# Performance work log

Measured on AMD Instinct MI355X. Metric: run time of the kernel, lower is better.

The kernel has to match this reference:

```python
import jax, jax.numpy as jnp
import numpy as np

ALPHA = 0.2  # LeakyReLU negative slope
NEG_INF = -9e15  # matches torch -9000000000000000.0


def setup_inputs() -> dict:
    key = jax.random.key(0)
    k1, k2, k3, k4, k5, k6 = jax.random.split(key, 6)
    N, F_in, F_out = 4096, 512, 256
    adj = jax.random.randint(k1, (N, N), 0, 2, dtype=jnp.int32)
    h = jax.random.normal(k2, (N, F_in), dtype=jnp.float32)
    # proj: Linear(F_in, F_out)
    W = jax.random.normal(k3, (F_in, F_out), dtype=jnp.float32) * (1.0 / np.sqrt(F_in))
    b = jax.random.normal(k4, (F_out,), dtype=jnp.float32) * 0.01
    # proj_a: Linear(2*F_out, 1) split into the two halves acting on src/dst features
    a1 = jax.random.normal(k5, (F_out,), dtype=jnp.float32) * (1.0 / np.sqrt(2 * F_out))
    a2 = jax.random.normal(k6, (F_out,), dtype=jnp.float32) * (1.0 / np.sqrt(2 * F_out))
    a_b = jnp.zeros((), dtype=jnp.float32)
    return {"adj": adj, "h": h, "W": W, "b": b, "a1": a1, "a2": a2, "a_b": a_b}


def reference(adj, h, W, b, a1, a2, a_b):
    # wh = proj(h): [N, F_out]
    wh = h @ W + b
    # Fused form of the N x N x 2F concat + Linear(2F,1):
    # logits[i, j] = wh[i] . a1 + wh[j] . a2 + a_b
    f_src = wh @ a1  # [N]
    f_dst = wh @ a2  # [N]
    e = jax.nn.leaky_relu(f_src[:, None] + f_dst[None, :] + a_b, negative_slope=ALPHA)
    e = jnp.where(adj > 0, e, NEG_INF)
    att = jax.nn.softmax(e, axis=-1)  # F.softmax legacy dim=1 for 2D
    # dropout: inference mode (no-op) for deterministic reference
    out = att @ wh  # [N, F_out]
    return jax.nn.elu(out)  # concat=True
```

## Files before the change

### kernel.cpp

```cpp
#include <hip/hip_runtime.h>

#define NN   4096
#define FIN  512
#define FOUT 256
#define ALPHA 0.2f

typedef __attribute__((ext_vector_type(8))) short short8;
typedef __attribute__((ext_vector_type(4))) float f32x4;
typedef unsigned short u16;

__device__ __forceinline__ u16 f2bf(float x) {
    union { float f; unsigned u; } v; v.f = x;
    unsigned r = v.u + 0x7FFF + ((v.u >> 16) & 1);
    return (u16)(r >> 16);
}

__global__ __launch_bounds__(256) void k_wt(const float* __restrict__ W,
                                            u16* __restrict__ Wt) {
    __shared__ float s[64 * 65];
    const int t  = threadIdx.x;
    const int f0 = blockIdx.x * 64;
    const int k0 = blockIdx.y * 64;
    #pragma unroll
    for (int p = 0; p < 4; ++p) {
        int q = t + 256 * p, rr = q >> 4, cc = q & 15;
        float4 w4 = *(const float4*)&W[(size_t)(k0 + rr) * FOUT + f0 + cc * 4];
        s[(cc * 4 + 0) * 65 + rr] = w4.x;
        s[(cc * 4 + 1) * 65 + rr] = w4.y;
        s[(cc * 4 + 2) * 65 + rr] = w4.z;
        s[(cc * 4 + 3) * 65 + rr] = w4.w;
    }
    __syncthreads();
    #pragma unroll
    for (int p = 0; p < 4; ++p) {
        int q = t + 256 * p, f = q >> 4, kg = q & 15;
        ushort4 o;
        o.x = f2bf(s[f * 65 + kg * 4 + 0]);
        o.y = f2bf(s[f * 65 + kg * 4 + 1]);
        o.z = f2bf(s[f * 65 + kg * 4 + 2]);
        o.w = f2bf(s[f * 65 + kg * 4 + 3]);
        *(ushort4*)&Wt[(size_t)(f0 + f) * FIN + k0 + kg * 4] = o;
    }
}

__global__ __launch_bounds__(256) void k_proj(const float* __restrict__ h,
                                              const u16* __restrict__ Wt,
                                              const float* __restrict__ bias,
                                              float* __restrict__ wh) {
    __shared__ u16 s_h[32 * 40];
    __shared__ u16 s_w[64 * 40];
    const int t  = threadIdx.x;
    const int i0 = blockIdx.y * 32;
    const int f0 = blockIdx.x * 64;
    const int wv = t >> 6, l = t & 63, n = l & 15, quad = l >> 4;
    const int m16 = (wv & 1) * 16, n32 = (wv >> 1) * 32;
    const int hr = t >> 3, hs = t & 7;
    const int wr = t >> 2, wg = t & 3;
    f32x4 acc[2] = {{0.f,0.f,0.f,0.f},{0.f,0.f,0.f,0.f}};
    for (int k0 = 0; k0 < FIN; k0 += 32) {
        __syncthreads();
        float4 hv = *(const float4*)&h[(size_t)(i0 + hr) * FIN + k0 + hs * 4];
        ushort4 hb; hb.x = f2bf(hv.x); hb.y = f2bf(hv.y); hb.z = f2bf(hv.z); hb.w = f2bf(hv.w);
        *(ushort4*)&s_h[hr * 40 + hs * 4] = hb;
        uint4 wvv = *(const uint4*)&Wt[(size_t)(f0 + wr) * FIN + k0 + wg * 8];
        *(uint4*)&s_w[wr * 40 + wg * 8] = wvv;
        __syncthreads();
        short8 a  = *(const short8*)&s_h[(m16 + n) * 40 + quad * 8];
        short8 b0 = *(const short8*)&s_w[(n32 + n) * 40 + quad * 8];
        short8 b1 = *(const short8*)&s_w[(n32 + 16 + n) * 40 + quad * 8];
        acc[0] = __builtin_amdgcn_mfma_f32_16x16x32_bf16(a, b0, acc[0], 0, 0, 0);
        acc[1] = __builtin_amdgcn_mfma_f32_16x16x32_bf16(a, b1, acc[1], 0, 0, 0);
    }
    #pragma unroll
    for (int u = 0; u < 2; ++u) {
        const int f = f0 + n32 + u * 16 + n;
        const float bv = bias[f];
        #pragma unroll
        for (int r = 0; r < 4; ++r) {
            const int i = i0 + m16 + quad * 4 + r;
            wh[(size_t)i * FOUT + f] = acc[u][r] + bv;
        }
    }
}

__global__ __launch_bounds__(64) void k_vec(const float* __restrict__ wh,
                                            const float* __restrict__ a1,
                                            const float* __restrict__ a2,
                                            const float* __restrict__ ab,
                                            float* __restrict__ fs,
                                            float* __restrict__ fd) {
    const int i = blockIdx.x;
    const int t = threadIdx.x;
    float4 w  = ((const float4*)(wh + (size_t)i * FOUT))[t];
    float4 v1 = ((const float4*)a1)[t];
    float4 v2 = ((const float4*)a2)[t];
    float d1 = w.x*v1.x + w.y*v1.y + w.z*v1.z + w.w*v1.w;
    float d2 = w.x*v2.x + w.y*v2.y + w.z*v2.z + w.w*v2.w;
    #pragma unroll
    for (int off = 32; off > 0; off >>= 1) {
        d1 += __shfl_down(d1, off);
        d2 += __shfl_down(d2, off);
    }
    if (t == 0) { fs[i] = d1 + ab[0]; fd[i] = d2; }
}

__global__ __launch_bounds__(256) void k_tr(const float* __restrict__ wh,
                                            u16* __restrict__ whT) {
    __shared__ float s[32 * 260];
    const int t = threadIdx.x;
    const int j0 = blockIdx.x * 32;
    #pragma unroll
    for (int p = 0; p < 8; ++p) {
        int q = t + 256 * p, j = q >> 6, f4 = q & 63;
        float4 v = *(const float4*)&wh[(size_t)(j0 + j) * FOUT + f4 * 4];
        *(float4*)&s[j * 260 + f4 * 4] = v;
    }
    __syncthreads();
    u16* dst = whT + (size_t)blockIdx.x * (FOUT * 32);
    #pragma unroll
    for (int p = 0; p < 8; ++p) {
        int q = t + 256 * p, f = q >> 3, jg = q & 7;
        ushort4 o;
        o.x = f2bf(s[(jg * 4 + 0) * 260 + f]);
        o.y = f2bf(s[(jg * 4 + 1) * 260 + f]);
        o.z = f2bf(s[(jg * 4 + 2) * 260 + f]);
        o.w = f2bf(s[(jg * 4 + 3) * 260 + f]);
        *(ushort4*)&dst[f * 32 + jg * 4] = o;
    }
}

#define BI 16
#define TJ 32
__global__ __launch_bounds__(256) void k_attn(const int* __restrict__ adj,
                                              const u16* __restrict__ whT,
                                              const float* __restrict__ fs,
                                              const float* __restrict__ fd,
                                              float* __restrict__ part,
                                              float* __restrict__ psum) {
    __shared__ u16   s_wt[256 * 40];
    __shared__ u16   s_p[BI * 40];
    __shared__ float s_fs[BI];
    __shared__ float s_red[TJ * BI];
    const int t  = threadIdx.x;
    const int i0 = blockIdx.x * BI;
    const int c  = blockIdx.y;
    const int jchunk = NN / gridDim.y;
    const int jbeg = c * jchunk, jend = jbeg + jchunk;
    const int jl = t & 31, rh = t >> 5;
    const int wv = t >> 6, l = t & 63, n = l & 15, quad = l >> 4;
    if (t < BI) s_fs[t] = fs[i0 + t];
    f32x4 acc[4] = {{0.f,0.f,0.f,0.f},{0.f,0.f,0.f,0.f},{0.f,0.f,0.f,0.f},{0.f,0.f,0.f,0.f}};
    float ps0 = 0.f, ps1 = 0.f;

    for (int j0 = jbeg; j0 < jend; j0 += TJ) {
        __syncthreads();
        float fdj = fd[j0 + jl];
        {
            int av = adj[(size_t)(i0 + rh) * NN + j0 + jl];
            float lg = s_fs[rh] + fdj;
            lg = lg > 0.f ? lg : ALPHA * lg;
            float p = (av > 0) ? __expf(lg) : 0.f;
            s_p[rh * 40 + jl] = f2bf(p); ps0 += p;
            int av2 = adj[(size_t)(i0 + rh + 8) * NN + j0 + jl];
            float lg2 = s_fs[rh + 8] + fdj;
            lg2 = lg2 > 0.f ? lg2 : ALPHA * lg2;
            float p2 = (av2 > 0) ? __expf(lg2) : 0.f;
            s_p[(rh + 8) * 40 + jl] = f2bf(p2); ps1 += p2;
        }
        const uint4* src = (const uint4*)(whT + (size_t)(j0 >> 5) * (FOUT * 32));
        #pragma unroll
        for (int p = 0; p < 4; ++p) {
            int q = t + 256 * p, f = q >> 2, sg = q & 3;
            uint4 v = src[q];
            *(uint4*)&s_wt[f * 40 + sg * 8] = v;
        }
        __syncthreads();
        short8 a = *(const short8*)&s_p[n * 40 + quad * 8];
        #pragma unroll
        for (int u = 0; u < 4; ++u) {
            short8 b = *(const short8*)&s_wt[(wv * 64 + u * 16 + n) * 40 + quad * 8];
            acc[u] = __builtin_amdgcn_mfma_f32_16x16x32_bf16(a, b, acc[u], 0, 0, 0);
        }
    }
    __syncthreads();
    s_red[jl * BI + rh]     = ps0;
    s_red[jl * BI + rh + 8] = ps1;
    __syncthreads();
    if (t < BI) {
        float sm = 0.f;
        #pragma unroll
        for (int jj = 0; jj < TJ; ++jj) sm += s_red[jj * BI + t];
        psum[(size_t)c * NN + i0 + t] = sm;
    }
    float* pc = part + ((size_t)c * NN + i0) * FOUT;
    #pragma unroll
    for (int u = 0; u < 4; ++u)
        #pragma unroll
        for (int r = 0; r < 4; ++r)
            pc[(size_t)(quad * 4 + r) * FOUT + wv * 64 + u * 16 + n] = acc[u][r];
}

__global__ __launch_bounds__(256) void k_comb(const float* __restrict__ part,
                                              const float* __restrict__ psum,
                                              float* __restrict__ out, int C) {
    const int g = blockIdx.x * 256 + threadIdx.x;
    const int i = g >> 6;
    const size_t s4 = (size_t)NN * FOUT / 4;
    float4 a = ((const float4*)part)[g];
    float s = psum[i];
    for (int c = 1; c < C; ++c) {
        float4 b = ((const float4*)part)[g + (size_t)c * s4];
        a.x += b.x; a.y += b.y; a.z += b.z; a.w += b.w;
        s += psum[(size_t)c * NN + i];
    }
    const float inv = 1.0f / s;
    a.x *= inv; a.y *= inv; a.z *= inv; a.w *= inv;
    a.x = a.x > 0.f ? a.x : __expf(a.x) - 1.f;
    a.y = a.y > 0.f ? a.y : __expf(a.y) - 1.f;
    a.z = a.z > 0.f ? a.z : __expf(a.z) - 1.f;
    a.w = a.w > 0.f ? a.w : __expf(a.w) - 1.f;
    ((float4*)out)[g] = a;
}

extern "C" void kernel_launch(void* const* d_in, const int* in_sizes, int n_in,
                              void* d_out, int out_size, void* d_ws, size_t ws_size,
                              hipStream_t stream) {
    const int*   adj = (const int*)  d_in[0];
    const float* h   = (const float*)d_in[1];
    const float* W   = (const float*)d_in[2];
    const float* b   = (const float*)d_in[3];
    const float* a1  = (const float*)d_in[4];
    const float* a2  = (const float*)d_in[5];
    const float* ab  = (const float*)d_in[6];
    float* out = (float*)d_out;

    auto need = [](int c) -> size_t {
        size_t fl = (size_t)NN * FOUT + 2 * NN + (size_t)c * NN + (size_t)c * NN * FOUT;
        size_t us = (size_t)FOUT * FIN + (size_t)NN * FOUT;
        return fl * 4 + us * 2;
    };
    int C = 8;
    while (C > 1 && need(C) > ws_size) C >>= 1;

    float* wh   = (float*)d_ws;
    float* fs   = wh + (size_t)NN * FOUT;
    float* fd   = fs + NN;
    float* psum = fd + NN;
    float* part = psum + (size_t)C * NN;
    u16*   Wt   = (u16*)(part + (size_t)C * NN * FOUT);
    u16*   whT  = Wt + (size_t)FOUT * FIN;

    k_wt  <<<dim3(FOUT / 64, FIN / 64), 256, 0, stream>>>(W, Wt);
    k_proj<<<dim3(FOUT / 64, NN / 32), 256, 0, stream>>>(h, Wt, b, wh);
    k_vec <<<NN, 64, 0, stream>>>(wh, a1, a2, ab, fs, fd);
    k_tr  <<<NN / 32, 256, 0, stream>>>(wh, whT);
    k_attn<<<dim3(NN / BI, C), 256, 0, stream>>>(adj, whT, fs, fd, part, psum);
    k_comb<<<(NN * FOUT / 4) / 256, 256, 0, stream>>>(part, psum, out, C);
}
```

Before: 180.6 us.

## Fuse transpose into projection, enlarge attention tiles, prefetch adj, read whT directly

The projection kernel now stages the whole h row-block in LDS once, reads W fragments straight from global memory, and writes the bf16 transposed whT tile itself, which removes the separate transpose kernel. k_vec packs four rows per block. The attention kernel doubles the row block to 32 and the j tile to 64. It also prefetches the next adjacency and fd values with vector loads, loads whT fragments straight from global memory instead of staging them in LDS, and reduces row sums with shuffles. The split count drops from 8 to 4, trading less partial-sum traffic for fewer blocks in flight.

New measurement: 151.3 us. 1.19x faster.

```diff
diff --git a/kernel.cpp b/kernel.cpp
--- a/kernel.cpp
+++ b/kernel.cpp
@@ -43,54 +43,58 @@
     }
 }
 
+#define HS 520
 __global__ __launch_bounds__(256) void k_proj(const float* __restrict__ h,
                                               const u16* __restrict__ Wt,
                                               const float* __restrict__ bias,
-                                              float* __restrict__ wh) {
-    __shared__ u16 s_h[32 * 40];
-    __shared__ u16 s_w[64 * 40];
+                                              float* __restrict__ wh,
+                                              u16* __restrict__ whT) {
+    __shared__ u16 s_h[32 * HS];
     const int t  = threadIdx.x;
+    const int f0 = blockIdx.x * 64;
     const int i0 = blockIdx.y * 32;
-    const int f0 = blockIdx.x * 64;
-    const int wv = t >> 6, l = t & 63, n = l & 15, quad = l >> 4;
-    const int m16 = (wv & 1) * 16, n32 = (wv >> 1) * 32;
-    const int hr = t >> 3, hs = t & 7;
-    const int wr = t >> 2, wg = t & 3;
+    #pragma unroll
+    for (int p = 0; p < 16; ++p) {
+        int q = t + 256 * p, row = q >> 7, c4 = q & 127;
+        float4 v = *(const float4*)&h[(size_t)(i0 + row) * FIN + c4 * 4];
+        ushort4 o; o.x = f2bf(v.x); o.y = f2bf(v.y); o.z = f2bf(v.z); o.w = f2bf(v.w);
+        *(ushort4*)&s_h[row * HS + c4 * 4] = o;
+    }
+    __syncthreads();
+    const int w = t >> 6, l = t & 63, n = l & 15, quad = l >> 4;
+    const int hh = w & 1, fh = w >> 1;
     f32x4 acc[2] = {{0.f,0.f,0.f,0.f},{0.f,0.f,0.f,0.f}};
+    #pragma unroll
     for (int k0 = 0; k0 < FIN; k0 += 32) {
-        __syncthreads();
-        float4 hv = *(const float4*)&h[(size_t)(i0 + hr) * FIN + k0 + hs * 4];
-        ushort4 hb; hb.x = f2bf(hv.x); hb.y = f2bf(hv.y); hb.z = f2bf(hv.z); hb.w = f2bf(hv.w);
-        *(ushort4*)&s_h[hr * 40 + hs * 4] = hb;
-        uint4 wvv = *(const uint4*)&Wt[(size_t)(f0 + wr) * FIN + k0 + wg * 8];
-        *(uint4*)&s_w[wr * 40 + wg * 8] = wvv;
-        __syncthreads();
-        short8 a  = *(const short8*)&s_h[(m16 + n) * 40 + quad * 8];
-        short8 b0 = *(const short8*)&s_w[(n32 + n) * 40 + quad * 8];
-        short8 b1 = *(const short8*)&s_w[(n32 + 16 + n) * 40 + quad * 8];
+        short8 a = *(const short8*)&s_h[(hh * 16 + n) * HS + k0 + quad * 8];
+        short8 b0 = *(const short8*)&Wt[(size_t)(f0 + fh * 32 + n) * FIN + k0 + quad * 8];
+        short8 b1 = *(const short8*)&Wt[(size_t)(f0 + fh * 32 + 16 + n) * FIN + k0 + quad * 8];
         acc[0] = __builtin_amdgcn_mfma_f32_16x16x32_bf16(a, b0, acc[0], 0, 0, 0);
         acc[1] = __builtin_amdgcn_mfma_f32_16x16x32_bf16(a, b1, acc[1], 0, 0, 0);
     }
+    u16* wt_tile = whT + (size_t)(i0 >> 5) * (FOUT * 32);
     #pragma unroll
     for (int u = 0; u < 2; ++u) {
-        const int f = f0 + n32 + u * 16 + n;
+        const int f = f0 + fh * 32 + u * 16 + n;
         const float bv = bias[f];
         #pragma unroll
         for (int r = 0; r < 4; ++r) {
-            const int i = i0 + m16 + quad * 4 + r;
-            wh[(size_t)i * FOUT + f] = acc[u][r] + bv;
-        }
-    }
-}
-
-__global__ __launch_bounds__(64) void k_vec(const float* __restrict__ wh,
-                                            const float* __restrict__ a1,
-                                            const float* __restrict__ a2,
-                                            const float* __restrict__ ab,
-                                            float* __restrict__ fs,
-                                            float* __restrict__ fd) {
-    const int i = blockIdx.x;
-    const int t = threadIdx.x;
+            const int i = i0 + hh * 16 + quad * 4 + r;
+            float val = acc[u][r] + bv;
+            wh[(size_t)i * FOUT + f] = val;
+            wt_tile[f * 32 + (i - i0)] = f2bf(val);
+        }
+    }
+}
+
+__global__ __launch_bounds__(256) void k_vec(const float* __restrict__ wh,
+                                             const float* __restrict__ a1,
+                                             const float* __restrict__ a2,
+                                             const float* __restrict__ ab,
+                                             float* __restrict__ fs,
+                                             float* __restrict__ fd) {
+    const int i = blockIdx.x * 4 + (threadIdx.x >> 6);
+    const int t = threadIdx.x & 63;
     float4 w  = ((const float4*)(wh + (size_t)i * FOUT))[t];
     float4 v1 = ((const float4*)a1)[t];
     float4 v2 = ((const float4*)a2)[t];
@@ -104,113 +108,104 @@
     if (t == 0) { fs[i] = d1 + ab[0]; fd[i] = d2; }
 }
 
-__global__ __launch_bounds__(256) void k_tr(const float* __restrict__ wh,
-                                            u16* __restrict__ whT) {
-    __shared__ float s[32 * 260];
-    const int t = threadIdx.x;
-    const int j0 = blockIdx.x * 32;
-    #pragma unroll
-    for (int p = 0; p < 8; ++p) {
-        int q = t + 256 * p, j = q >> 6, f4 = q & 63;
-        float4 v = *(const float4*)&wh[(size_t)(j0 + j) * FOUT + f4 * 4];
-        *(float4*)&s[j * 260 + f4 * 4] = v;
-    }
-    __syncthreads();
-    u16* dst = whT + (size_t)blockIdx.x * (FOUT * 32);
-    #pragma unroll
-    for (int p = 0; p < 8; ++p) {
-        int q = t + 256 * p, f = q >> 3, jg = q & 7;
-        ushort4 o;
-        o.x = f2bf(s[(jg * 4 + 0) * 260 + f]);
-        o.y = f2bf(s[(jg * 4 + 1) * 260 + f]);
-        o.z = f2bf(s[(jg * 4 + 2) * 260 + f]);
-        o.w = f2bf(s[(jg * 4 + 3) * 260 + f]);
-        *(ushort4*)&dst[f * 32 + jg * 4] = o;
-    }
-}
-
-#define BI 16
-#define TJ 32
+#define BI 32
+#define TJ 64
+#define PS 72
 __global__ __launch_bounds__(256) void k_attn(const int* __restrict__ adj,
                                               const u16* __restrict__ whT,
                                               const float* __restrict__ fs,
                                               const float* __restrict__ fd,
                                               float* __restrict__ part,
                                               float* __restrict__ psum) {
-    __shared__ u16   s_wt[256 * 40];
-    __shared__ u16   s_p[BI * 40];
-    __shared__ float s_fs[BI];
-    __shared__ float s_red[TJ * BI];
+    __shared__ u16 s_p[BI * PS];
     const int t  = threadIdx.x;
     const int i0 = blockIdx.x * BI;
     const int c  = blockIdx.y;
     const int jchunk = NN / gridDim.y;
     const int jbeg = c * jchunk, jend = jbeg + jchunk;
-    const int jl = t & 31, rh = t >> 5;
-    const int wv = t >> 6, l = t & 63, n = l & 15, quad = l >> 4;
-    if (t < BI) s_fs[t] = fs[i0 + t];
-    f32x4 acc[4] = {{0.f,0.f,0.f,0.f},{0.f,0.f,0.f,0.f},{0.f,0.f,0.f,0.f},{0.f,0.f,0.f,0.f}};
-    float ps0 = 0.f, ps1 = 0.f;
+    const int jq = t & 15, rh = t >> 4;
+    const float fs0 = fs[i0 + rh], fs1 = fs[i0 + rh + 16];
+    const int w = t >> 6, l = t & 63, n = l & 15, quad = l >> 4;
+
+    f32x4 acc[2][4] = {{{0.f,0.f,0.f,0.f},{0.f,0.f,0.f,0.f},{0.f,0.f,0.f,0.f},{0.f,0.f,0.f,0.f}},
+                       {{0.f,0.f,0.f,0.f},{0.f,0.f,0.f,0.f},{0.f,0.f,0.f,0.f},{0.f,0.f,0.f,0.f}}};
+    float rs0 = 0.f, rs1 = 0.f;
+
+    int4   av0 = *(const int4*)&adj[(size_t)(i0 + rh) * NN + jbeg + jq * 4];
+    int4   av1 = *(const int4*)&adj[(size_t)(i0 + rh + 16) * NN + jbeg + jq * 4];
+    float4 fdv = *(const float4*)&fd[jbeg + jq * 4];
 
     for (int j0 = jbeg; j0 < jend; j0 += TJ) {
+        ushort4 o0, o1;
+        {
+            float x, p;
+            x = fs0 + fdv.x; x = x > 0.f ? x : ALPHA * x; p = av0.x > 0 ? __expf(x) : 0.f; o0.x = f2bf(p); rs0 += p;
+            x = fs0 + fdv.y; x = x > 0.f ? x : ALPHA * x; p = av0.y > 0 ? __expf(x) : 0.f; o0.y = f2bf(p); rs0 += p;
+            x = fs0 + fdv.z; x = x > 0.f ? x : ALPHA * x; p = av0.z > 0 ? __expf(x) : 0.f; o0.z = f2bf(p); rs0 += p;
+            x = fs0 + fdv.w; x = x > 0.f ? x : ALPHA * x; p = av0.w > 0 ? __expf(x) : 0.f; o0.w = f2bf(p); rs0 += p;
+            x = fs1 + fdv.x; x = x > 0.f ? x : ALPHA * x; p = av1.x > 0 ? __expf(x) : 0.f; o1.x = f2bf(p); rs1 += p;
+            x = fs1 + fdv.y; x = x > 0.f ? x : ALPHA * x; p = av1.y > 0 ? __expf(x) : 0.f; o1.y = f2bf(p); rs1 += p;
+            x = fs1 + fdv.z; x = x > 0.f ? x : ALPHA * x; p = av1.z > 0 ? __expf(x) : 0.f; o1.z = f2bf(p); rs1 += p;
+            x = fs1 + fdv.w; x = x > 0.f ? x : ALPHA * x; p = av1.w > 0 ? __expf(x) : 0.f; o1.w = f2bf(p); rs1 += p;
+        }
         __syncthreads();
-        float fdj = fd[j0 + jl];
-        {
-            int av = adj[(size_t)(i0 + rh) * NN + j0 + jl];
-            float lg = s_fs[rh] + fdj;
-            lg = lg > 0.f ? lg : ALPHA * lg;
-            float p = (av > 0) ? __expf(lg) : 0.f;
-            s_p[rh * 40 + jl] = f2bf(p); ps0 += p;
-            int av2 = adj[(size_t)(i0 + rh + 8) * NN + j0 + jl];
-            float lg2 = s_fs[rh + 8] + fdj;
-            lg2 = lg2 > 0.f ? lg2 : ALPHA * lg2;
-            float p2 = (av2 > 0) ? __expf(lg2) : 0.f;
-            s_p[(rh + 8) * 40 + jl] = f2bf(p2); ps1 += p2;
-        }
-        const uint4* src = (const uint4*)(whT + (size_t)(j0 >> 5) * (FOUT * 32));
-        #pragma unroll
-        for (int p = 0; p < 4; ++p) {
-            int q = t + 256 * p, f = q >> 2, sg = q & 3;
-            uint4 v = src[q];
-            *(uint4*)&s_wt[f * 40 + sg * 8] = v;
+        *(ushort4*)&s_p[rh * PS + jq * 4]        = o0;
+        *(ushort4*)&s_p[(rh + 16) * PS + jq * 4] = o1;
+        if (j0 + TJ < jend) {
+            av0 = *(const int4*)&adj[(size_t)(i0 + rh) * NN + j0 + TJ + jq * 4];
+            av1 = *(const int4*)&adj[(size_t)(i0 + rh + 16) * NN + j0 + TJ + jq * 4];
+            fdv = *(const float4*)&fd[j0 + TJ + jq * 4];
+        }
+        short8 b[2][4];
+        #pragma unroll
+        for (int s = 0; s < 2; ++s) {
+            const u16* tb = whT + (size_t)((j0 >> 5) + s) * (FOUT * 32) + quad * 8;
+            #pragma unroll
+            for (int u = 0; u < 4; ++u)
+                b[s][u] = *(const short8*)&tb[(w * 64 + u * 16 + n) * 32];
         }
         __syncthreads();
-        short8 a = *(const short8*)&s_p[n * 40 + quad * 8];
-        #pragma unroll
-        for (int u = 0; u < 4; ++u) {
-            short8 b = *(const short8*)&s_wt[(wv * 64 + u * 16 + n) * 40 + quad * 8];
-            acc[u] = __builtin_amdgcn_mfma_f32_16x16x32_bf16(a, b, acc[u], 0, 0, 0);
-        }
-    }
-    __syncthreads();
-    s_red[jl * BI + rh]     = ps0;
-    s_red[jl * BI + rh + 8] = ps1;
-    __syncthreads();
-    if (t < BI) {
-        float sm = 0.f;
-        #pragma unroll
-        for (int jj = 0; jj < TJ; ++jj) sm += s_red[jj * BI + t];
-        psum[(size_t)c * NN + i0 + t] = sm;
+        #pragma unroll
+        for (int s = 0; s < 2; ++s) {
+            short8 a0 = *(const short8*)&s_p[n * PS + s * 32 + quad * 8];
+            short8 a1f = *(const short8*)&s_p[(16 + n) * PS + s * 32 + quad * 8];
+            #pragma unroll
+            for (int u = 0; u < 4; ++u) {
+                acc[0][u] = __builtin_amdgcn_mfma_f32_16x16x32_bf16(a0,  b[s][u], acc[0][u], 0, 0, 0);
+                acc[1][u] = __builtin_amdgcn_mfma_f32_16x16x32_bf16(a1f, b[s][u], acc[1][u], 0, 0, 0);
+            }
+        }
+    }
+    #pragma unroll
+    for (int m = 8; m > 0; m >>= 1) {
+        rs0 += __shfl_xor(rs0, m);
+        rs1 += __shfl_xor(rs1, m);
+    }
+    if (jq == 0) {
+        psum[(size_t)c * NN + i0 + rh]      = rs0;
+        psum[(size_t)c * NN + i0 + rh + 16] = rs1;
     }
     float* pc = part + ((size_t)c * NN + i0) * FOUT;
     #pragma unroll
-    for (int u = 0; u < 4; ++u)
-        #pragma unroll
-        for (int r = 0; r < 4; ++r)
-            pc[(size_t)(quad * 4 + r) * FOUT + wv * 64 + u * 16 + n] = acc[u][r];
-}
-
-__global__ __launch_bounds__(256) void k_comb(const float* __restrict__ part,
-                                              const float* __restrict__ psum,
-                                              float* __restrict__ out, int C) {
+    for (int hf = 0; hf < 2; ++hf)
+        #pragma unroll
+        for (int u = 0; u < 4; ++u)
+            #pragma unroll
+            for (int r = 0; r < 4; ++r)
+                pc[(size_t)(hf * 16 + quad * 4 + r) * FOUT + w * 64 + u * 16 + n] = acc[hf][u][r];
+}
+
+__global__ __launch_bounds__(256) void k_fin(const float* __restrict__ part,
+                                             const float* __restrict__ psum,
+                                             float* __restrict__ out, int C) {
     const int g = blockIdx.x * 256 + threadIdx.x;
     const int i = g >> 6;
     const size_t s4 = (size_t)NN * FOUT / 4;
     float4 a = ((const float4*)part)[g];
     float s = psum[i];
     for (int c = 1; c < C; ++c) {
-        float4 b = ((const float4*)part)[g + (size_t)c * s4];
-        a.x += b.x; a.y += b.y; a.z += b.z; a.w += b.w;
+        float4 bb = ((const float4*)part)[g + (size_t)c * s4];
+        a.x += bb.x; a.y += bb.y; a.z += bb.z; a.w += bb.w;
         s += psum[(size_t)c * NN + i];
     }
     const float inv = 1.0f / s;
@@ -239,7 +234,7 @@
         size_t us = (size_t)FOUT * FIN + (size_t)NN * FOUT;
         return fl * 4 + us * 2;
     };
-    int C = 8;
+    int C = 4;
     while (C > 1 && need(C) > ws_size) C >>= 1;
 
     float* wh   = (float*)d_ws;
@@ -251,9 +246,8 @@
     u16*   whT  = Wt + (size_t)FOUT * FIN;
 
     k_wt  <<<dim3(FOUT / 64, FIN / 64), 256, 0, stream>>>(W, Wt);
-    k_proj<<<dim3(FOUT / 64, NN / 32), 256, 0, stream>>>(h, Wt, b, wh);
-    k_vec <<<NN, 64, 0, stream>>>(wh, a1, a2, ab, fs, fd);
-    k_tr  <<<NN / 32, 256, 0, stream>>>(wh, whT);
+    k_proj<<<dim3(FOUT / 64, NN / 32), 256, 0, stream>>>(h, Wt, b, wh, whT);
+    k_vec <<<NN / 4, 256, 0, stream>>>(wh, a1, a2, ab, fs, fd);
     k_attn<<<dim3(NN / BI, C), 256, 0, stream>>>(adj, whT, fs, fd, part, psum);
-    k_comb<<<(NN * FOUT / 4) / 256, 256, 0, stream>>>(part, psum, out, C);
-}
+    k_fin <<<(NN * FOUT / 4) / 256, 256, 0, stream>>>(part, psum, out, C);
+}
```
